# Kernel tuning notes

Measured on AMD Instinct MI355X. Metric: run time of the kernel, lower is better.

The kernel has to match this reference:

```python
import jax, jax.numpy as jnp
import numpy as np


def _run_lstm(x, h0, c0, Wih, Whh, bih, bhh):
    """Batched single-layer unidirectional LSTM (PyTorch gate order i,f,g,o).
    x: [B,T,D]; h0,c0: [B,H]; Wih: [4H,D]; Whh: [4H,H]. Returns ys [B,T,H], hT, cT."""
    def step(carry, xt):
        h, c = carry
        g = xt @ Wih.T + h @ Whh.T + bih + bhh  # [B,4H]
        i, f, gg, o = jnp.split(g, 4, axis=-1)
        c = jax.nn.sigmoid(f) * c + jax.nn.sigmoid(i) * jnp.tanh(gg)
        h = jax.nn.sigmoid(o) * jnp.tanh(c)
        return (h, c), h
    (hT, cT), ys = jax.lax.scan(step, (h0, c0), jnp.swapaxes(x, 0, 1))
    return jnp.swapaxes(ys, 0, 1), hT, cT


def setup_inputs() -> dict:
    key = jax.random.key(0)
    ks = jax.random.split(key, 16)
    B, T, D, H, L, V = 16, 256, 512, 1024, 512, 32000
    s = 0.05
    return {
        "x": jax.random.normal(ks[0], (B, T, D), jnp.float32),
        "eps": jax.random.normal(ks[1], (B, L), jnp.float32),
        "enc_Wih": jax.random.normal(ks[2], (4 * H, D), jnp.float32) * s,
        "enc_Whh": jax.random.normal(ks[3], (4 * H, H), jnp.float32) * s,
        "enc_bih": jax.random.normal(ks[4], (4 * H,), jnp.float32) * s,
        "enc_bhh": jax.random.normal(ks[5], (4 * H,), jnp.float32) * s,
        "Wmu": jax.random.normal(ks[6], (L, H), jnp.float32) * s,
        "bmu": jax.random.normal(ks[7], (L,), jnp.float32) * s,
        "Wlv": jax.random.normal(ks[8], (L, H), jnp.float32) * s,
        "blv": jax.random.normal(ks[9], (L,), jnp.float32) * s,
        "dec_Wih": jax.random.normal(ks[10], (4 * L, D), jnp.float32) * s,
        "dec_Whh": jax.random.normal(ks[11], (4 * L, L), jnp.float32) * s,
        "dec_bih": jax.random.normal(ks[12], (4 * L,), jnp.float32) * s,
        "dec_bhh": jax.random.normal(ks[13], (4 * L,), jnp.float32) * s,
        "Wout": jax.random.normal(ks[14], (V, L), jnp.float32) * s,
        "bout": jax.random.normal(ks[15], (V,), jnp.float32) * s,
    }


def reference(x, eps, enc_Wih, enc_Whh, enc_bih, enc_bhh, Wmu, bmu, Wlv, blv,
              dec_Wih, dec_Whh, dec_bih, dec_bhh, Wout, bout):
    B, T, D = x.shape
    H = enc_Whh.shape[1]
    L = Wmu.shape[0]
    # --- encode (equal-length sequences => per-sample loop == one batched LSTM) ---
    h0 = jnp.zeros((B, H), x.dtype)
    _, hT, _ = _run_lstm(x, h0, h0, enc_Wih, enc_Whh, enc_bih, enc_bhh)  # hT: [B,H]
    mu = jax.nn.relu(hT @ Wmu.T + bmu)          # [B,L]
    logvar = jax.nn.relu(hT @ Wlv.T + blv)      # [B,L]
    # --- reparameterize ---
    z = eps * jnp.exp(0.5 * logvar) + mu        # [B,L]
    # --- decode: teacher forcing, inputs shifted right by one (zeros prepended) ---
    dec_in = jnp.concatenate([jnp.zeros((B, 1, D), x.dtype), x[:, :-1]], axis=1)
    c0 = jnp.zeros((B, L), x.dtype)
    ys, _, _ = _run_lstm(dec_in, z, c0, dec_Wih, dec_Whh, dec_bih, dec_bhh)  # [B,T,L]
    logits = ys @ Wout.T + bout                 # [B,T,V]
    recons = jax.nn.softmax(logits, axis=-1)
    # match torch shapes: mus/logvars/z are [B, 1(layer), 1(per-sample batch), L]
    z4 = z[:, None, None, :]
    mu4 = mu[:, None, None, :]
    lv4 = logvar[:, None, None, :]
    return recons, z4, mu4, lv4
```

## Files before the change

kernel.cpp:

```cpp
#include <hip/hip_runtime.h>
#include <hip/hip_bf16.h>
#include <stdint.h>

#define NSLOT 32
#define GRID_LSTM 512

typedef __attribute__((ext_vector_type(4))) float f32x4;
typedef __attribute__((ext_vector_type(4))) int   i32x4;
typedef __attribute__((ext_vector_type(8))) __bf16 bf16x8;
typedef __attribute__((ext_vector_type(8))) unsigned short u16x8;

__device__ __forceinline__ float sigf(float x) { return 1.f / (1.f + __expf(-x)); }
__device__ __forceinline__ float tanhf_fast(float x) { return 1.f - 2.f / (__expf(2.f * x) + 1.f); }

__device__ __forceinline__ unsigned short f2bf(float f) {
    union { __hip_bfloat16 h; unsigned short u; } cv;
    cv.h = __float2bfloat16(f);
    return cv.u;
}
__device__ __forceinline__ float bf2f(unsigned short u) {
    union { float f; unsigned v; } c; c.v = ((unsigned)u) << 16; return c.f;
}

#define QP(x, c) __int_as_float(__builtin_amdgcn_mov_dpp(__float_as_int(x), (c), 0xF, 0xF, true))

__device__ __forceinline__ unsigned long long pack4(unsigned int h16) {
    unsigned int o4 = (unsigned int)__shfl_xor((int)h16, 4, 64);
    unsigned int p1 = h16 | (o4 << 16);
    unsigned int p2 = (unsigned int)__shfl_xor((int)p1, 8, 64);
    return (unsigned long long)p1 | ((unsigned long long)p2 << 32);
}

__device__ __forceinline__ bf16x8 load16_sc0(const unsigned short* p) {
    bf16x8 r;
    asm volatile("global_load_dwordx4 %0, %1, off sc0" : "=v"(r) : "v"(p));
    return r;
}

__device__ __forceinline__ void gld_lds16(const unsigned short* g, unsigned short* l) {
    __builtin_amdgcn_global_load_lds(
        (const __attribute__((address_space(1))) unsigned int*)g,
        (__attribute__((address_space(3))) unsigned int*)l, 16, 0, 0);
}

__device__ __forceinline__ void flag_arrive(unsigned* flags, int slot, unsigned target, int tid) {
    asm volatile("s_waitcnt vmcnt(0)" ::: "memory");
    __syncthreads();
    if (tid == 0)
        __hip_atomic_store(&flags[slot * 16], target, __ATOMIC_RELAXED, __HIP_MEMORY_SCOPE_AGENT);
}
__device__ __forceinline__ void flag_wait(unsigned* flags, unsigned target, int tid) {
    if (tid < NSLOT) {
        long sp = 0;
        while (__hip_atomic_load(&flags[tid * 16], __ATOMIC_RELAXED, __HIP_MEMORY_SCOPE_AGENT) < target) {
            if (++sp > (1L << 20)) break;
        }
    }
    __syncthreads();
    __builtin_amdgcn_sched_barrier(0);
    asm volatile("" ::: "memory");
}

__device__ __forceinline__ void register_block(unsigned* regcnt, int* s_slot, int* s_xcd, int tid) {
    if (tid == 0) {
        unsigned x;
        asm volatile("s_getreg_b32 %0, hwreg(HW_REG_XCC_ID)" : "=s"(x));
        x &= 7u;
        unsigned my = __hip_atomic_fetch_add(&regcnt[x * 16], 1u,
                                             __ATOMIC_RELAXED, __HIP_MEMORY_SCOPE_AGENT);
        *s_xcd = (int)x;
        *s_slot = (my < NSLOT) ? (int)my : -1;
    }
    __syncthreads();
}

#define CTRL_DWORDS (128 + 128 + 4096 + 4096)
__global__ void init_kernel(unsigned* ctrl) {
    int id = blockIdx.x * 256 + threadIdx.x;
    if (id < CTRL_DWORDS)
        __hip_atomic_store(&ctrl[id], 0u, __ATOMIC_RELAXED, __HIP_MEMORY_SCOPE_AGENT);
}

__global__ __launch_bounds__(256) void cvt_f32_bf16(const float* __restrict__ w,
                                                    unsigned short* __restrict__ o, int n4) {
    int id = blockIdx.x * 256 + threadIdx.x;
    if (id >= n4) return;
    f32x4 v = *(const f32x4*)(w + (size_t)id * 4);
    ushort4 r;
    r.x = f2bf(v.x); r.y = f2bf(v.y); r.z = f2bf(v.z); r.w = f2bf(v.w);
    *(ushort4*)(o + (size_t)id * 4) = r;
}

__global__ __launch_bounds__(256) void gemm_gx(
        const unsigned short* __restrict__ A, const unsigned short* __restrict__ Bm,
        unsigned short* __restrict__ outb, int N) {
    __shared__ __align__(16) unsigned short lA[128 * 32];
    __shared__ __align__(16) unsigned short lB[128 * 32];
    const int tid = threadIdx.x, bid = blockIdx.x;
    const int mt = bid & 31, nt = bid >> 5;
    const int m0 = mt * 128, n0 = nt * 128;
    const int lane = tid & 63, wvv = tid >> 6;
    const int wm = wvv >> 1, wn = wvv & 1;
    const int sr = tid >> 2, sc = (tid & 3) * 8;
    const int fr = lane & 15, kc = (lane >> 4) * 8;
    unsigned short* ldsA0 = lA + wvv * 512;
    unsigned short* ldsA1 = lA + 2048 + wvv * 512;
    unsigned short* ldsB0 = lB + wvv * 512;
    unsigned short* ldsB1 = lB + 2048 + wvv * 512;
    f32x4 acc[4][4];
    #pragma unroll
    for (int i = 0; i < 4; ++i)
        #pragma unroll
        for (int j = 0; j < 4; ++j) acc[i][j] = f32x4{0.f, 0.f, 0.f, 0.f};
    for (int k0 = 0; k0 < 512; k0 += 32) {
        __syncthreads();
        gld_lds16(A  + (size_t)(m0 + sr) * 512 + k0 + sc,        ldsA0);
        gld_lds16(A  + (size_t)(m0 + sr + 64) * 512 + k0 + sc,   ldsA1);
        gld_lds16(Bm + (size_t)(n0 + sr) * 512 + k0 + sc,        ldsB0);
        gld_lds16(Bm + (size_t)(n0 + sr + 64) * 512 + k0 + sc,   ldsB1);
        __syncthreads();
        bf16x8 af[4], bfr[4];
        #pragma unroll
        for (int mi = 0; mi < 4; ++mi)
            af[mi] = *(const bf16x8*)(lA + (wm * 64 + mi * 16 + fr) * 32 + kc);
        #pragma unroll
        for (int ni = 0; ni < 4; ++ni)
            bfr[ni] = *(const bf16x8*)(lB + (wn * 64 + ni * 16 + fr) * 32 + kc);
        #pragma unroll
        for (int mi = 0; mi < 4; ++mi)
            #pragma unroll
            for (int ni = 0; ni < 4; ++ni)
                acc[mi][ni] = __builtin_amdgcn_mfma_f32_16x16x32_bf16(af[mi], bfr[ni], acc[mi][ni], 0, 0, 0);
    }
    const int orow = (lane >> 4) * 4;
    #pragma unroll
    for (int mi = 0; mi < 4; ++mi)
        #pragma unroll
        for (int ni = 0; ni < 4; ++ni) {
            int gm = m0 + wm * 64 + mi * 16 + orow;
            int gn = n0 + wn * 64 + ni * 16 + fr;
            #pragma unroll
            for (int j = 0; j < 4; ++j)
                outb[(size_t)(gm + j) * N + gn] = f2bf(acc[mi][ni][j]);
        }
}

__global__ __launch_bounds__(256, 1) void enc_kernel(
        const float* __restrict__ Whh, const float* __restrict__ bih, const float* __restrict__ bhh,
        const unsigned short* __restrict__ gxe ,
        unsigned short* ring_e, float* __restrict__ hT, unsigned* ctrl) {
    __shared__ int s_slot, s_xcd;
    const int tid = threadIdx.x;
    register_block(ctrl , &s_slot, &s_xcd, tid);
    const int slot = s_slot, xcd = s_xcd;
    if (slot < 0) return;
    unsigned* flags = ctrl + 256 + (size_t)xcd * NSLOT * 16;
    unsigned short* ringg = ring_e + (size_t)xcd * 2 * 16384;

    const int l = tid & 63, wv = tid >> 6;
    const int n = l & 15;
    const int kch = (l >> 4) * 8;
    const int ub = slot * 32 + wv * 8;
    const int colA = (n & 3) * 1024 + ub + (n >> 2);
    const int colB = colA + 4;
    bf16x8 wA[32], wB[32];
    #pragma unroll
    for (int kk = 0; kk < 32; ++kk) {
        {
            const float* src = Whh + (size_t)colA * 1024 + kk * 32 + kch;
            f32x4 w0 = *(const f32x4*)src, w1 = *(const f32x4*)(src + 4);
            union { bf16x8 v; unsigned short u[8]; } cv;
            cv.u[0] = f2bf(w0.x); cv.u[1] = f2bf(w0.y); cv.u[2] = f2bf(w0.z); cv.u[3] = f2bf(w0.w);
            cv.u[4] = f2bf(w1.x); cv.u[5] = f2bf(w1.y); cv.u[6] = f2bf(w1.z); cv.u[7] = f2bf(w1.w);
            wA[kk] = cv.v;
        }
        {
            const float* src = Whh + (size_t)colB * 1024 + kk * 32 + kch;
            f32x4 w0 = *(const f32x4*)src, w1 = *(const f32x4*)(src + 4);
            union { bf16x8 v; unsigned short u[8]; } cv;
            cv.u[0] = f2bf(w0.x); cv.u[1] = f2bf(w0.y); cv.u[2] = f2bf(w0.z); cv.u[3] = f2bf(w0.w);
            cv.u[4] = f2bf(w1.x); cv.u[5] = f2bf(w1.y); cv.u[6] = f2bf(w1.z); cv.u[7] = f2bf(w1.w);
            wB[kk] = cv.v;
        }
    }
    const float biasA = bih[colA] + bhh[colA];
    const float biasB = bih[colB] + bhh[colB];
    float cA0 = 0.f, cA1 = 0.f, cA2 = 0.f, cA3 = 0.f;
    float cB0 = 0.f, cB1 = 0.f, cB2 = 0.f, cB3 = 0.f;
    const bool b0 = (l & 1), b1 = (l & 2);
    const bool g0lane = ((l & 3) == 0);
    const int batbase = (l >> 4) * 4;
    for (int t = 0; t < 256; ++t) {
        float gA0, gA1, gA2, gA3, gB0, gB1, gB2, gB3;
        {
            const unsigned short* g0p = gxe + ((size_t)(batbase + 0) * 256 + t) * 4096;
            const unsigned short* g1p = gxe + ((size_t)(batbase + 1) * 256 + t) * 4096;
            const unsigned short* g2p = gxe + ((size_t)(batbase + 2) * 256 + t) * 4096;
            const unsigned short* g3p = gxe + ((size_t)(batbase + 3) * 256 + t) * 4096;
            gA0 = bf2f(g0p[colA]); gB0 = bf2f(g0p[colB]);
            gA1 = bf2f(g1p[colA]); gB1 = bf2f(g1p[colB]);
            gA2 = bf2f(g2p[colA]); gB2 = bf2f(g2p[colB]);
            gA3 = bf2f(g3p[colA]); gB3 = bf2f(g3p[colB]);
        }
        f32x4 aA0 = {0.f,0.f,0.f,0.f}, aA1 = {0.f,0.f,0.f,0.f};
        f32x4 aB0 = {0.f,0.f,0.f,0.f}, aB1 = {0.f,0.f,0.f,0.f};
        if (t > 0) {
            flag_wait(flags, (unsigned)t, tid);
            const unsigned short* hb = ringg + ((t - 1) & 1) * 16384 + n * 32 + kch;
            bf16x8 ha[32];
            #pragma unroll
            for (int kk = 0; kk < 32; ++kk) ha[kk] = load16_sc0(hb + kk * 512);
            asm volatile("s_waitcnt vmcnt(0)" ::: "memory");
            __builtin_amdgcn_sched_barrier(0);
            #pragma unroll
            for (int kk = 0; kk < 16; ++kk) {
                aA0 = __builtin_amdgcn_mfma_f32_16x16x32_bf16(ha[kk],      wA[kk],      aA0, 0, 0, 0);
                aB0 = __builtin_amdgcn_mfma_f32_16x16x32_bf16(ha[kk],      wB[kk],      aB0, 0, 0, 0);
                aA1 = __builtin_amdgcn_mfma_f32_16x16x32_bf16(ha[kk + 16], wA[16 + kk], aA1, 0, 0, 0);
                aB1 = __builtin_amdgcn_mfma_f32_16x16x32_bf16(ha[kk + 16], wB[16 + kk], aB1, 0, 0, 0);
            }
        }
        unsigned short* sw = ringg + (t & 1) * 16384 + slot * 512 + wv * 8;
        #pragma unroll
        for (int j = 0; j < 4; ++j) {
            float gAj = (j == 0) ? gA0 : (j == 1) ? gA1 : (j == 2) ? gA2 : gA3;
            float gBj = (j == 0) ? gB0 : (j == 1) ? gB1 : (j == 2) ? gB2 : gB3;
            int bat = batbase + j;
            {
                float v = aA0[j] + aA1[j] + gAj + biasA;
                float vx1 = QP(v, 0xB1), vx2 = QP(v, 0x4E), vx3 = QP(v, 0x1B);
                float iv = b1 ? (b0 ? vx3 : vx2) : (b0 ? vx1 : v);
                float fv = b1 ? (b0 ? vx2 : vx3) : (b0 ? v   : vx1);
                float gv = b1 ? (b0 ? vx1 : v  ) : (b0 ? vx3 : vx2);
                float ov = b1 ? (b0 ? v   : vx1) : (b0 ? vx2 : vx3);
                float cj = (j == 0) ? cA0 : (j == 1) ? cA1 : (j == 2) ? cA2 : cA3;
                float cn = sigf(fv) * cj + sigf(iv) * tanhf_fast(gv);
                if (j == 0) cA0 = cn; else if (j == 1) cA1 = cn; else if (j == 2) cA2 = cn; else cA3 = cn;
                float h = sigf(ov) * tanhf_fast(cn);
                unsigned long long pk = pack4((unsigned)f2bf(h));
                if ((l & 15) == 0) *(unsigned long long*)(sw + bat * 32) = pk;
                if (g0lane && xcd == 0 && t == 255) hT[bat * 1024 + ub + (n >> 2)] = h;
            }
            {
                float v = aB0[j] + aB1[j] + gBj + biasB;
                float vx1 = QP(v, 0xB1), vx2 = QP(v, 0x4E), vx3 = QP(v, 0x1B);
                float iv = b1 ? (b0 ? vx3 : vx2) : (b0 ? vx1 : v);
                float fv = b1 ? (b0 ? vx2 : vx3) : (b0 ? v   : vx1);
                float gv = b1 ? (b0 ? vx1 : v  ) : (b0 ? vx3 : vx2);
                float ov = b1 ? (b0 ? v   : vx1) : (b0 ? vx2 : vx3);
                float cj = (j == 0) ? cB0 : (j == 1) ? cB1 : (j == 2) ? cB2 : cB3;
                float cn = sigf(fv) * cj + sigf(iv) * tanhf_fast(gv);
                if (j == 0) cB0 = cn; else if (j == 1) cB1 = cn; else if (j == 2) cB2 = cn; else cB3 = cn;
                float h = sigf(ov) * tanhf_fast(cn);
                unsigned long long pk = pack4((unsigned)f2bf(h));
                if ((l & 15) == 0) *(unsigned long long*)(sw + bat * 32 + 4) = pk;
                if (g0lane && xcd == 0 && t == 255) hT[bat * 1024 + ub + 4 + (n >> 2)] = h;
            }
        }
        flag_arrive(flags, slot, (unsigned)(t + 1), tid);
    }
}

__global__ __launch_bounds__(256) void mlz_kernel(
        const float* __restrict__ hT, const float* __restrict__ Wmu, const float* __restrict__ bmu,
        const float* __restrict__ Wlv, const float* __restrict__ blv, const float* __restrict__ eps,
        unsigned short* __restrict__ z_ring, float* __restrict__ out_tail) {
    int id = blockIdx.x * 256 + threadIdx.x;
    int l = id & 511, b = id >> 9;
    const float* hb = hT + b * 1024;
    const float* wm = Wmu + (size_t)l * 1024;
    const float* wl = Wlv + (size_t)l * 1024;
    float am = 0.f, al = 0.f;
    for (int k = 0; k < 256; ++k) {
        f32x4 h4 = *(const f32x4*)(hb + k * 4);
        f32x4 m4 = *(const f32x4*)(wm + k * 4);
        f32x4 l4 = *(const f32x4*)(wl + k * 4);
        am += m4.x * h4.x + m4.y * h4.y + m4.z * h4.z + m4.w * h4.w;
        al += l4.x * h4.x + l4.y * h4.y + l4.z * h4.z + l4.w * h4.w;
    }
    float mu = fmaxf(am + bmu[l], 0.f);
    float lv = fmaxf(al + blv[l], 0.f);
    float z  = eps[id] * __expf(0.5f * lv) + mu;
    z_ring[(l >> 4) * 256 + b * 16 + (l & 15)] = f2bf(z);
    out_tail[id] = z;
    out_tail[8192 + id] = mu;
    out_tail[16384 + id] = lv;
}

__global__ __launch_bounds__(256, 1) void dec_kernel(
        const float* __restrict__ Wih, const float* __restrict__ Whh,
        const float* __restrict__ bih, const float* __restrict__ bhh,
        const unsigned short* __restrict__ x_bf, const unsigned short* __restrict__ z_ring,
        unsigned short* ring_d, unsigned short* __restrict__ ys_bf, unsigned* ctrl) {
    __shared__ int s_slot, s_xcd;
    const int tid = threadIdx.x;
    register_block(ctrl + 128 , &s_slot, &s_xcd, tid);
    const int slot = s_slot, xcd = s_xcd;
    if (slot < 0) return;
    unsigned* flags = ctrl + 256 + 4096 + (size_t)xcd * NSLOT * 16;
    unsigned short* ringg = ring_d + (size_t)xcd * 2 * 8192;

    const int l = tid & 63, wv = tid >> 6;
    const int n = l & 15;
    const int kch = (l >> 4) * 8;
    const int ub = slot * 16 + wv * 4;
    const int col = (n & 3) * 512 + ub + (n >> 2);
    bf16x8 wf[32];
    #pragma unroll
    for (int kk = 0; kk < 32; ++kk) {
        const float* src = (kk < 16) ? (Wih + (size_t)col * 512 + kk * 32 + kch)
                                     : (Whh + (size_t)col * 512 + (kk - 16) * 32 + kch);
        f32x4 w0 = *(const f32x4*)src, w1 = *(const f32x4*)(src + 4);
        union { bf16x8 v; unsigned short u[8]; } cv;
        cv.u[0] = f2bf(w0.x); cv.u[1] = f2bf(w0.y); cv.u[2] = f2bf(w0.z); cv.u[3] = f2bf(w0.w);
        cv.u[4] = f2bf(w1.x); cv.u[5] = f2bf(w1.y); cv.u[6] = f2bf(w1.z); cv.u[7] = f2bf(w1.w);
        wf[kk] = cv.v;
    }
    const float bias = bih[col] + bhh[col];
    float c0 = 0.f, c1 = 0.f, c2 = 0.f, c3 = 0.f;
    const bool b0 = (l & 1), b1 = (l & 2);
    const bool g0lane = ((l & 3) == 0);
    const int batbase = (l >> 4) * 4;
    for (int t = 0; t < 256; ++t) {
        f32x4 acc0 = {0.f,0.f,0.f,0.f}, acc1 = {0.f,0.f,0.f,0.f};
        if (t > 0) {
            const unsigned short* xrow = x_bf + ((size_t)n * 256 + (t - 1)) * 512 + kch;
            #pragma unroll
            for (int kk = 0; kk < 16; ++kk) {
                bf16x8 a = *(const bf16x8*)(xrow + kk * 32);
                acc0 = __builtin_amdgcn_mfma_f32_16x16x32_bf16(a, wf[kk], acc0, 0, 0, 0);
            }
            flag_wait(flags, (unsigned)t, tid);
        }
        bf16x8 ha[16];
        if (t == 0) {
            #pragma unroll
            for (int kk = 0; kk < 16; ++kk) {
                int k = kk * 32 + kch;
                ha[kk] = *(const bf16x8*)(z_ring + (k >> 4) * 256 + n * 16 + (k & 15));
            }
        } else {
            const unsigned short* base = ringg + ((t - 1) & 1) * 8192;
            #pragma unroll
            for (int kk = 0; kk < 16; ++kk) {
                int k = kk * 32 + kch;
                ha[kk] = load16_sc0(base + (k >> 4) * 256 + n * 16 + (k & 15));
            }
            asm volatile("s_waitcnt vmcnt(0)" ::: "memory");
            __builtin_amdgcn_sched_barrier(0);
        }
        #pragma unroll
        for (int kk = 0; kk < 8; ++kk) {
            acc0 = __builtin_amdgcn_mfma_f32_16x16x32_bf16(ha[kk],     wf[16 + kk], acc0, 0, 0, 0);
            acc1 = __builtin_amdgcn_mfma_f32_16x16x32_bf16(ha[kk + 8], wf[24 + kk], acc1, 0, 0, 0);
        }
        unsigned short* sw = ringg + (t & 1) * 8192 + slot * 256 + wv * 4;
        #pragma unroll
        for (int j = 0; j < 4; ++j) {
            float v   = acc0[j] + acc1[j] + bias;
            float vx1 = QP(v, 0xB1), vx2 = QP(v, 0x4E), vx3 = QP(v, 0x1B);
            float iv = b1 ? (b0 ? vx3 : vx2) : (b0 ? vx1 : v);
            float fv = b1 ? (b0 ? vx2 : vx3) : (b0 ? v   : vx1);
            float gv = b1 ? (b0 ? vx1 : v  ) : (b0 ? vx3 : vx2);
            float ov = b1 ? (b0 ? v   : vx1) : (b0 ? vx2 : vx3);
            float cj = (j == 0) ? c0 : (j == 1) ? c1 : (j == 2) ? c2 : c3;
            float cn = sigf(fv) * cj + sigf(iv) * tanhf_fast(gv);
            if (j == 0) c0 = cn; else if (j == 1) c1 = cn; else if (j == 2) c2 = cn; else c3 = cn;
            float h = sigf(ov) * tanhf_fast(cn);
            unsigned long long pk = pack4((unsigned)f2bf(h));
            int bat = batbase + j;
            if ((l & 15) == 0) *(unsigned long long*)(sw + bat * 16) = pk;
            if (g0lane && xcd == 0)
                ys_bf[((size_t)bat * 256 + t) * 512 + ub + (n >> 2)] = f2bf(h);
        }
        flag_arrive(flags, slot, (unsigned)(t + 1), tid);
    }
}

__global__ __launch_bounds__(256) void gemm_logits(
        const unsigned short* __restrict__ A, const unsigned short* __restrict__ Wb,
        const float* __restrict__ bout, float* __restrict__ out,
        unsigned short* __restrict__ lgbf, int bfmode) {
    __shared__ __align__(16) unsigned short lA[128 * 32];
    __shared__ __align__(16) unsigned short lB[128 * 32];
    const int tid = threadIdx.x, bid = blockIdx.x;
    const int mt = bid & 31, nt = bid >> 5;
    const int m0 = mt * 128, n0 = nt * 128;
    const int lane = tid & 63, wvv = tid >> 6;
    const int wm = wvv >> 1, wn = wvv & 1;
    const int sr = tid >> 2, sc = (tid & 3) * 8;
    const int fr = lane & 15, kc = (lane >> 4) * 8;
    unsigned short* ldsA0 = lA + wvv * 512;
    unsigned short* ldsA1 = lA + 2048 + wvv * 512;
    unsigned short* ldsB0 = lB + wvv * 512;
    unsigned short* ldsB1 = lB + 2048 + wvv * 512;
    f32x4 acc[4][4];
    #pragma unroll
    for (int i = 0; i < 4; ++i)
        #pragma unroll
        for (int j = 0; j < 4; ++j) acc[i][j] = f32x4{0.f, 0.f, 0.f, 0.f};
    for (int k0 = 0; k0 < 512; k0 += 32) {
        __syncthreads();
        gld_lds16(A  + (size_t)(m0 + sr) * 512 + k0 + sc,        ldsA0);
        gld_lds16(A  + (size_t)(m0 + sr + 64) * 512 + k0 + sc,   ldsA1);
        gld_lds16(Wb + (size_t)(n0 + sr) * 512 + k0 + sc,        ldsB0);
        gld_lds16(Wb + (size_t)(n0 + sr + 64) * 512 + k0 + sc,   ldsB1);
        __syncthreads();
        bf16x8 af[4], bfr[4];
        #pragma unroll
        for (int mi = 0; mi < 4; ++mi)
            af[mi] = *(const bf16x8*)(lA + (wm * 64 + mi * 16 + fr) * 32 + kc);
        #pragma unroll
        for (int ni = 0; ni < 4; ++ni)
            bfr[ni] = *(const bf16x8*)(lB + (wn * 64 + ni * 16 + fr) * 32 + kc);
        #pragma unroll
        for (int mi = 0; mi < 4; ++mi)
            #pragma unroll
            for (int ni = 0; ni < 4; ++ni)
                acc[mi][ni] = __builtin_amdgcn_mfma_f32_16x16x32_bf16(af[mi], bfr[ni], acc[mi][ni], 0, 0, 0);
    }
    const int orow = (lane >> 4) * 4;
    #pragma unroll
    for (int mi = 0; mi < 4; ++mi)
        #pragma unroll
        for (int ni = 0; ni < 4; ++ni) {
            int gm = m0 + wm * 64 + mi * 16 + orow;
            int gn = n0 + wn * 64 + ni * 16 + fr;
            float bo = bout[gn];
            if (bfmode) {
                #pragma unroll
                for (int j = 0; j < 4; ++j)
                    lgbf[(size_t)(gm + j) * 32000 + gn] = f2bf(acc[mi][ni][j] + bo);
            } else {
                #pragma unroll
                for (int j = 0; j < 4; ++j)
                    out[(size_t)(gm + j) * 32000 + gn] = acc[mi][ni][j] + bo;
            }
        }
}

__global__ __launch_bounds__(512) void softmax_kernel(float* __restrict__ out) {
    __shared__ __align__(16) float row[32000];
    __shared__ float red[8];
    const int tid = threadIdx.x;
    float* p = out + (size_t)blockIdx.x * 32000;
    float mx = -3.4e38f;
    for (int c = tid; c < 8000; c += 512) {
        f32x4 v = *(const f32x4*)(p + c * 4);
        *(f32x4*)(row + c * 4) = v;
        mx = fmaxf(mx, fmaxf(fmaxf(v.x, v.y), fmaxf(v.z, v.w)));
    }
    #pragma unroll
    for (int o = 32; o; o >>= 1) mx = fmaxf(mx, __shfl_xor(mx, o, 64));
    if ((tid & 63) == 0) red[tid >> 6] = mx;
    __syncthreads();
    if (tid == 0) {
        float m = red[0];
        for (int i = 1; i < 8; ++i) m = fmaxf(m, red[i]);
        red[0] = m;
    }
    __syncthreads();
    mx = red[0];
    __syncthreads();
    float s = 0.f;
    for (int c = tid; c < 8000; c += 512) {
        f32x4 v = *(f32x4*)(row + c * 4);
        v.x = __expf(v.x - mx); v.y = __expf(v.y - mx);
        v.z = __expf(v.z - mx); v.w = __expf(v.w - mx);
        *(f32x4*)(row + c * 4) = v;
        s += v.x + v.y + v.z + v.w;
    }
    #pragma unroll
    for (int o = 32; o; o >>= 1) s += __shfl_xor(s, o, 64);
    if ((tid & 63) == 0) red[tid >> 6] = s;
    __syncthreads();
    if (tid == 0) {
        float t2 = 0.f;
        for (int i = 0; i < 8; ++i) t2 += red[i];
        red[0] = t2;
    }
    __syncthreads();
    float inv = 1.f / red[0];
    for (int c = tid; c < 8000; c += 512) {
        f32x4 v = *(f32x4*)(row + c * 4);
        v.x *= inv; v.y *= inv; v.z *= inv; v.w *= inv;
        *(f32x4*)(p + c * 4) = v;
    }
}

__global__ __launch_bounds__(512) void softmax_bf16(const unsigned short* __restrict__ lgbf,
                                                    float* __restrict__ out) {
    __shared__ __align__(16) float row[32000];
    __shared__ float red[8];
    const int tid = threadIdx.x;
    const unsigned short* lp = lgbf + (size_t)blockIdx.x * 32000;
    float* p = out + (size_t)blockIdx.x * 32000;
    float mx = -3.4e38f;
    for (int c = tid; c < 4000; c += 512) {
        u16x8 v = *(const u16x8*)(lp + c * 8);
        #pragma unroll
        for (int q = 0; q < 8; ++q) {
            float f = bf2f(v[q]);
            row[c * 8 + q] = f;
            mx = fmaxf(mx, f);
        }
    }
    #pragma unroll
    for (int o = 32; o; o >>= 1) mx = fmaxf(mx, __shfl_xor(mx, o, 64));
    if ((tid & 63) == 0) red[tid >> 6] = mx;
    __syncthreads();
    if (tid == 0) {
        float m = red[0];
        for (int i = 1; i < 8; ++i) m = fmaxf(m, red[i]);
        red[0] = m;
    }
    __syncthreads();
    mx = red[0];
    __syncthreads();
    float s = 0.f;
    for (int c = tid; c < 8000; c += 512) {
        f32x4 v = *(f32x4*)(row + c * 4);
        v.x = __expf(v.x - mx); v.y = __expf(v.y - mx);
        v.z = __expf(v.z - mx); v.w = __expf(v.w - mx);
        *(f32x4*)(row + c * 4) = v;
        s += v.x + v.y + v.z + v.w;
    }
    #pragma unroll
    for (int o = 32; o; o >>= 1) s += __shfl_xor(s, o, 64);
    if ((tid & 63) == 0) red[tid >> 6] = s;
    __syncthreads();
    if (tid == 0) {
        float t2 = 0.f;
        for (int i = 0; i < 8; ++i) t2 += red[i];
        red[0] = t2;
    }
    __syncthreads();
    float inv = 1.f / red[0];
    for (int c = tid; c < 8000; c += 512) {
        f32x4 v = *(f32x4*)(row + c * 4);
        v.x *= inv; v.y *= inv; v.z *= inv; v.w *= inv;
        *(f32x4*)(p + c * 4) = v;
    }
}

extern "C" void kernel_launch(void* const* d_in, const int* in_sizes, int n_in,
                              void* d_out, int out_size, void* d_ws, size_t ws_size,
                              hipStream_t stream) {
    (void)in_sizes; (void)n_in; (void)out_size;
    const float* x    = (const float*)d_in[0];
    const float* eps  = (const float*)d_in[1];
    const float* eWih = (const float*)d_in[2];
    const float* eWhh = (const float*)d_in[3];
    const float* ebih = (const float*)d_in[4];
    const float* ebhh = (const float*)d_in[5];
    const float* Wmu  = (const float*)d_in[6];
    const float* bmu  = (const float*)d_in[7];
    const float* Wlv  = (const float*)d_in[8];
    const float* blv  = (const float*)d_in[9];
    const float* dWih = (const float*)d_in[10];
    const float* dWhh = (const float*)d_in[11];
    const float* dbih = (const float*)d_in[12];
    const float* dbhh = (const float*)d_in[13];
    const float* Wout = (const float*)d_in[14];
    const float* bout = (const float*)d_in[15];
    float* out = (float*)d_out;

    char* ws = (char*)d_ws;
    unsigned* ctrl         = (unsigned*)ws;
    unsigned short* x_bf   = (unsigned short*)(ws + 65536);
    unsigned short* ysbf   = x_bf + (size_t)16 * 256 * 512;
    unsigned short* ring_e = ysbf + (size_t)4096 * 512;
    unsigned short* ring_d = ring_e + (size_t)8 * 2 * 16384;
    unsigned short* z_ring = ring_d + (size_t)8 * 2 * 8192;
    float* hT              = (float*)(z_ring + 8192);
    unsigned short* gxe    = (unsigned short*)(hT + 16384);
    unsigned short* wih_bf = ysbf;
    unsigned short* wo_bf  = gxe;
    const size_t base_end  = 65536 + 4194304 + 4194304 + 524288 + 262144 + 16384 + 65536 + 33554432;
    const size_t lg_bytes  = (size_t)4096 * 32000 * 2;
    const int bfmode       = (ws_size >= base_end + lg_bytes) ? 1 : 0;
    unsigned short* lg_bf  = (unsigned short*)(ws + base_end);

    hipLaunchKernelGGL(init_kernel, dim3(33), dim3(256), 0, stream, ctrl);
    hipLaunchKernelGGL(cvt_f32_bf16, dim3(2048), dim3(256), 0, stream, x, x_bf, 524288);
    hipLaunchKernelGGL(cvt_f32_bf16, dim3(2048), dim3(256), 0, stream, eWih, wih_bf, 524288);
    hipLaunchKernelGGL(gemm_gx, dim3(1024), dim3(256), 0, stream, x_bf, wih_bf, gxe, 4096);
    hipLaunchKernelGGL(enc_kernel, dim3(GRID_LSTM), dim3(256), 0, stream,
                       eWhh, ebih, ebhh, gxe, ring_e, hT, ctrl);
    hipLaunchKernelGGL(cvt_f32_bf16, dim3(16000), dim3(256), 0, stream, Wout, wo_bf, 4096000);
    hipLaunchKernelGGL(mlz_kernel, dim3(32), dim3(256), 0, stream,
                       hT, Wmu, bmu, Wlv, blv, eps, z_ring, out + 131072000);
    hipLaunchKernelGGL(dec_kernel, dim3(GRID_LSTM), dim3(256), 0, stream,
                       dWih, dWhh, dbih, dbhh, x_bf, z_ring, ring_d, ysbf, ctrl);
    hipLaunchKernelGGL(gemm_logits, dim3(8000), dim3(256), 0, stream,
                       ysbf, wo_bf, bout, out, lg_bf, bfmode);
    if (bfmode)
        hipLaunchKernelGGL(softmax_bf16, dim3(4096), dim3(512), 0, stream, lg_bf, out);
    else
        hipLaunchKernelGGL(softmax_kernel, dim3(4096), dim3(512), 0, stream, out);
}
```

Baseline: 3.404 ms.

## Double LSTM block width, halve slots, and convert Wout in idle blocks

```diff
diff --git a/kernel.cpp b/kernel.cpp
--- a/kernel.cpp
+++ b/kernel.cpp
@@ -2,7 +2,8 @@
 #include <hip/hip_bf16.h>
 #include <stdint.h>
 
-#define NSLOT 32
+#define NSLOT 16
+#define TPB_LSTM 512
 #define GRID_LSTM 512
 
 typedef __attribute__((ext_vector_type(4))) float f32x4;
@@ -79,6 +80,18 @@
     int id = blockIdx.x * 256 + threadIdx.x;
     if (id < CTRL_DWORDS)
         __hip_atomic_store(&ctrl[id], 0u, __ATOMIC_RELAXED, __HIP_MEMORY_SCOPE_AGENT);
+}
+
+__global__ __launch_bounds__(256) void cvt_x_wih(const float* __restrict__ x, unsigned short* __restrict__ xb,
+                                                 const float* __restrict__ w, unsigned short* __restrict__ wb) {
+    int id = blockIdx.x * 256 + threadIdx.x;
+    const float* src; unsigned short* dst; int i;
+    if (id < 524288) { src = x; dst = xb; i = id; }
+    else             { src = w; dst = wb; i = id - 524288; }
+    f32x4 v = *(const f32x4*)(src + (size_t)i * 4);
+    ushort4 r;
+    r.x = f2bf(v.x); r.y = f2bf(v.y); r.z = f2bf(v.z); r.w = f2bf(v.w);
+    *(ushort4*)(dst + (size_t)i * 4) = r;
 }
 
 __global__ __launch_bounds__(256) void cvt_f32_bf16(const float* __restrict__ w,
@@ -145,22 +158,44 @@
         }
 }
 
-__global__ __launch_bounds__(256, 1) void enc_kernel(
+__global__ __launch_bounds__(TPB_LSTM, 1) void enc_kernel(
         const float* __restrict__ Whh, const float* __restrict__ bih, const float* __restrict__ bhh,
         const unsigned short* __restrict__ gxe ,
-        unsigned short* ring_e, float* __restrict__ hT, unsigned* ctrl) {
+        unsigned short* ring_e, float* __restrict__ hT, unsigned* ctrl,
+        const float* __restrict__ Wout, unsigned short* __restrict__ wo_bf, int bfmode) {
     __shared__ int s_slot, s_xcd;
+    __shared__ int s_chunk;
     const int tid = threadIdx.x;
     register_block(ctrl , &s_slot, &s_xcd, tid);
     const int slot = s_slot, xcd = s_xcd;
-    if (slot < 0) return;
-    unsigned* flags = ctrl + 256 + (size_t)xcd * NSLOT * 16;
+    if (slot < 0) {
+        if (!bfmode) return;
+        for (;;) {
+            if (tid == 0)
+                s_chunk = (int)__hip_atomic_fetch_add(&ctrl[1], 1u,
+                                                      __ATOMIC_RELAXED, __HIP_MEMORY_SCOPE_AGENT);
+            __syncthreads();
+            int chunk = s_chunk;
+            __syncthreads();
+            if (chunk >= 1000) break;
+            size_t base = (size_t)chunk * 4096;
+            for (int i = tid; i < 4096; i += TPB_LSTM) {
+                size_t idx = base + i;
+                f32x4 v = *(const f32x4*)(Wout + idx * 4);
+                ushort4 r;
+                r.x = f2bf(v.x); r.y = f2bf(v.y); r.z = f2bf(v.z); r.w = f2bf(v.w);
+                *(ushort4*)(wo_bf + idx * 4) = r;
+            }
+        }
+        return;
+    }
+    unsigned* flags = ctrl + 256 + (size_t)xcd * 32 * 16;
     unsigned short* ringg = ring_e + (size_t)xcd * 2 * 16384;
 
     const int l = tid & 63, wv = tid >> 6;
     const int n = l & 15;
     const int kch = (l >> 4) * 8;
-    const int ub = slot * 32 + wv * 8;
+    const int ub = slot * 64 + wv * 8;
     const int colA = (n & 3) * 1024 + ub + (n >> 2);
     const int colB = colA + 4;
     bf16x8 wA[32], wB[32];
@@ -206,10 +241,13 @@
         f32x4 aB0 = {0.f,0.f,0.f,0.f}, aB1 = {0.f,0.f,0.f,0.f};
         if (t > 0) {
             flag_wait(flags, (unsigned)t, tid);
-            const unsigned short* hb = ringg + ((t - 1) & 1) * 16384 + n * 32 + kch;
+            const unsigned short* hb = ringg + ((t - 1) & 1) * 16384;
             bf16x8 ha[32];
             #pragma unroll
-            for (int kk = 0; kk < 32; ++kk) ha[kk] = load16_sc0(hb + kk * 512);
+            for (int kk = 0; kk < 32; ++kk) {
+                int ku = kk * 32 + kch;
+                ha[kk] = load16_sc0(hb + (ku >> 6) * 1024 + n * 64 + (ku & 63));
+            }
             asm volatile("s_waitcnt vmcnt(0)" ::: "memory");
             __builtin_amdgcn_sched_barrier(0);
             #pragma unroll
@@ -220,7 +258,7 @@
                 aB1 = __builtin_amdgcn_mfma_f32_16x16x32_bf16(ha[kk + 16], wB[16 + kk], aB1, 0, 0, 0);
             }
         }
-        unsigned short* sw = ringg + (t & 1) * 16384 + slot * 512 + wv * 8;
+        unsigned short* sw = ringg + (t & 1) * 16384 + slot * 1024 + wv * 8;
         #pragma unroll
         for (int j = 0; j < 4; ++j) {
             float gAj = (j == 0) ? gA0 : (j == 1) ? gA1 : (j == 2) ? gA2 : gA3;
@@ -238,7 +276,7 @@
                 if (j == 0) cA0 = cn; else if (j == 1) cA1 = cn; else if (j == 2) cA2 = cn; else cA3 = cn;
                 float h = sigf(ov) * tanhf_fast(cn);
                 unsigned long long pk = pack4((unsigned)f2bf(h));
-                if ((l & 15) == 0) *(unsigned long long*)(sw + bat * 32) = pk;
+                if ((l & 15) == 0) *(unsigned long long*)(sw + bat * 64) = pk;
                 if (g0lane && xcd == 0 && t == 255) hT[bat * 1024 + ub + (n >> 2)] = h;
             }
             {
@@ -253,7 +291,7 @@
                 if (j == 0) cB0 = cn; else if (j == 1) cB1 = cn; else if (j == 2) cB2 = cn; else cB3 = cn;
                 float h = sigf(ov) * tanhf_fast(cn);
                 unsigned long long pk = pack4((unsigned)f2bf(h));
-                if ((l & 15) == 0) *(unsigned long long*)(sw + bat * 32 + 4) = pk;
+                if ((l & 15) == 0) *(unsigned long long*)(sw + bat * 64 + 4) = pk;
                 if (g0lane && xcd == 0 && t == 255) hT[bat * 1024 + ub + 4 + (n >> 2)] = h;
             }
         }
@@ -281,13 +319,13 @@
     float mu = fmaxf(am + bmu[l], 0.f);
     float lv = fmaxf(al + blv[l], 0.f);
     float z  = eps[id] * __expf(0.5f * lv) + mu;
-    z_ring[(l >> 4) * 256 + b * 16 + (l & 15)] = f2bf(z);
+    z_ring[(l >> 5) * 512 + b * 32 + (l & 31)] = f2bf(z);
     out_tail[id] = z;
     out_tail[8192 + id] = mu;
     out_tail[16384 + id] = lv;
 }
 
-__global__ __launch_bounds__(256, 1) void dec_kernel(
+__global__ __launch_bounds__(TPB_LSTM, 1) void dec_kernel(
         const float* __restrict__ Wih, const float* __restrict__ Whh,
         const float* __restrict__ bih, const float* __restrict__ bhh,
         const unsigned short* __restrict__ x_bf, const unsigned short* __restrict__ z_ring,
@@ -297,13 +335,13 @@
     register_block(ctrl + 128 , &s_slot, &s_xcd, tid);
     const int slot = s_slot, xcd = s_xcd;
     if (slot < 0) return;
-    unsigned* flags = ctrl + 256 + 4096 + (size_t)xcd * NSLOT * 16;
+    unsigned* flags = ctrl + 256 + 4096 + (size_t)xcd * 32 * 16;
     unsigned short* ringg = ring_d + (size_t)xcd * 2 * 8192;
 
     const int l = tid & 63, wv = tid >> 6;
     const int n = l & 15;
     const int kch = (l >> 4) * 8;
-    const int ub = slot * 16 + wv * 4;
+    const int ub = slot * 32 + wv * 4;
     const int col = (n & 3) * 512 + ub + (n >> 2);
     bf16x8 wf[32];
     #pragma unroll
@@ -335,17 +373,13 @@
         bf16x8 ha[16];
         if (t == 0) {
             #pragma unroll
-            for (int kk = 0; kk < 16; ++kk) {
-                int k = kk * 32 + kch;
-                ha[kk] = *(const bf16x8*)(z_ring + (k >> 4) * 256 + n * 16 + (k & 15));
-            }
+            for (int kk = 0; kk < 16; ++kk)
+                ha[kk] = *(const bf16x8*)(z_ring + kk * 512 + n * 32 + kch);
         } else {
             const unsigned short* base = ringg + ((t - 1) & 1) * 8192;
             #pragma unroll
-            for (int kk = 0; kk < 16; ++kk) {
-                int k = kk * 32 + kch;
-                ha[kk] = load16_sc0(base + (k >> 4) * 256 + n * 16 + (k & 15));
-            }
+            for (int kk = 0; kk < 16; ++kk)
+                ha[kk] = load16_sc0(base + kk * 512 + n * 32 + kch);
             asm volatile("s_waitcnt vmcnt(0)" ::: "memory");
             __builtin_amdgcn_sched_barrier(0);
         }
@@ -354,7 +388,7 @@
             acc0 = __builtin_amdgcn_mfma_f32_16x16x32_bf16(ha[kk],     wf[16 + kk], acc0, 0, 0, 0);
             acc1 = __builtin_amdgcn_mfma_f32_16x16x32_bf16(ha[kk + 8], wf[24 + kk], acc1, 0, 0, 0);
         }
-        unsigned short* sw = ringg + (t & 1) * 8192 + slot * 256 + wv * 4;
+        unsigned short* sw = ringg + (t & 1) * 8192 + slot * 512 + wv * 4;
         #pragma unroll
         for (int j = 0; j < 4; ++j) {
             float v   = acc0[j] + acc1[j] + bias;
@@ -369,7 +403,7 @@
             float h = sigf(ov) * tanhf_fast(cn);
             unsigned long long pk = pack4((unsigned)f2bf(h));
             int bat = batbase + j;
-            if ((l & 15) == 0) *(unsigned long long*)(sw + bat * 16) = pk;
+            if ((l & 15) == 0) *(unsigned long long*)(sw + bat * 32) = pk;
             if (g0lane && xcd == 0)
                 ys_bf[((size_t)bat * 256 + t) * 512 + ub + (n >> 2)] = f2bf(h);
         }
@@ -575,22 +609,22 @@
     float* hT              = (float*)(z_ring + 8192);
     unsigned short* gxe    = (unsigned short*)(hT + 16384);
     unsigned short* wih_bf = ysbf;
-    unsigned short* wo_bf  = gxe;
     const size_t base_end  = 65536 + 4194304 + 4194304 + 524288 + 262144 + 16384 + 65536 + 33554432;
     const size_t lg_bytes  = (size_t)4096 * 32000 * 2;
     const int bfmode       = (ws_size >= base_end + lg_bytes) ? 1 : 0;
     unsigned short* lg_bf  = (unsigned short*)(ws + base_end);
+    unsigned short* wo_bf  = bfmode ? (unsigned short*)(out + (size_t)100000000) : gxe;
 
     hipLaunchKernelGGL(init_kernel, dim3(33), dim3(256), 0, stream, ctrl);
-    hipLaunchKernelGGL(cvt_f32_bf16, dim3(2048), dim3(256), 0, stream, x, x_bf, 524288);
-    hipLaunchKernelGGL(cvt_f32_bf16, dim3(2048), dim3(256), 0, stream, eWih, wih_bf, 524288);
+    hipLaunchKernelGGL(cvt_x_wih, dim3(4096), dim3(256), 0, stream, x, x_bf, eWih, wih_bf);
     hipLaunchKernelGGL(gemm_gx, dim3(1024), dim3(256), 0, stream, x_bf, wih_bf, gxe, 4096);
-    hipLaunchKernelGGL(enc_kernel, dim3(GRID_LSTM), dim3(256), 0, stream,
-                       eWhh, ebih, ebhh, gxe, ring_e, hT, ctrl);
-    hipLaunchKernelGGL(cvt_f32_bf16, dim3(16000), dim3(256), 0, stream, Wout, wo_bf, 4096000);
+    hipLaunchKernelGGL(enc_kernel, dim3(GRID_LSTM), dim3(TPB_LSTM), 0, stream,
+                       eWhh, ebih, ebhh, gxe, ring_e, hT, ctrl, Wout, wo_bf, bfmode);
+    if (!bfmode)
+        hipLaunchKernelGGL(cvt_f32_bf16, dim3(16000), dim3(256), 0, stream, Wout, wo_bf, 4096000);
     hipLaunchKernelGGL(mlz_kernel, dim3(32), dim3(256), 0, stream,
                        hT, Wmu, bmu, Wlv, blv, eps, z_ring, out + 131072000);
-    hipLaunchKernelGGL(dec_kernel, dim3(GRID_LSTM), dim3(256), 0, stream,
+    hipLaunchKernelGGL(dec_kernel, dim3(GRID_LSTM), dim3(TPB_LSTM), 0, stream,
                        dWih, dWhh, dbih, dbhh, x_bf, z_ring, ring_d, ysbf, ctrl);
     hipLaunchKernelGGL(gemm_logits, dim3(8000), dim3(256), 0, stream,
                        ysbf, wo_bf, bout, out, lg_bf, bfmode);
```

After: 8.794 ms. +158.4%, slower.

## Overlap Wout bf16 conversion with encoder LSTM using idle blocks

Applied to the files above, without the earlier changes.

```diff
diff --git a/kernel.cpp b/kernel.cpp
--- a/kernel.cpp
+++ b/kernel.cpp
@@ -79,6 +79,18 @@
     int id = blockIdx.x * 256 + threadIdx.x;
     if (id < CTRL_DWORDS)
         __hip_atomic_store(&ctrl[id], 0u, __ATOMIC_RELAXED, __HIP_MEMORY_SCOPE_AGENT);
+}
+
+__global__ __launch_bounds__(256) void cvt_x_wih(const float* __restrict__ x, unsigned short* __restrict__ xb,
+                                                 const float* __restrict__ w, unsigned short* __restrict__ wb) {
+    int id = blockIdx.x * 256 + threadIdx.x;
+    const float* src; unsigned short* dst; int i;
+    if (id < 524288) { src = x; dst = xb; i = id; }
+    else             { src = w; dst = wb; i = id - 524288; }
+    f32x4 v = *(const f32x4*)(src + (size_t)i * 4);
+    ushort4 r;
+    r.x = f2bf(v.x); r.y = f2bf(v.y); r.z = f2bf(v.z); r.w = f2bf(v.w);
+    *(ushort4*)(dst + (size_t)i * 4) = r;
 }
 
 __global__ __launch_bounds__(256) void cvt_f32_bf16(const float* __restrict__ w,
@@ -148,12 +160,34 @@
 __global__ __launch_bounds__(256, 1) void enc_kernel(
         const float* __restrict__ Whh, const float* __restrict__ bih, const float* __restrict__ bhh,
         const unsigned short* __restrict__ gxe ,
-        unsigned short* ring_e, float* __restrict__ hT, unsigned* ctrl) {
+        unsigned short* ring_e, float* __restrict__ hT, unsigned* ctrl,
+        const float* __restrict__ Wout, unsigned short* __restrict__ wo_bf, int bfmode) {
     __shared__ int s_slot, s_xcd;
+    __shared__ int s_chunk;
     const int tid = threadIdx.x;
     register_block(ctrl , &s_slot, &s_xcd, tid);
     const int slot = s_slot, xcd = s_xcd;
-    if (slot < 0) return;
+    if (slot < 0) {
+        if (!bfmode) return;
+        for (;;) {
+            if (tid == 0)
+                s_chunk = (int)__hip_atomic_fetch_add(&ctrl[1], 1u,
+                                                      __ATOMIC_RELAXED, __HIP_MEMORY_SCOPE_AGENT);
+            __syncthreads();
+            int chunk = s_chunk;
+            __syncthreads();
+            if (chunk >= 1000) break;
+            size_t base = (size_t)chunk * 4096;
+            for (int i = tid; i < 4096; i += 256) {
+                size_t idx = base + i;
+                f32x4 v = *(const f32x4*)(Wout + idx * 4);
+                ushort4 r;
+                r.x = f2bf(v.x); r.y = f2bf(v.y); r.z = f2bf(v.z); r.w = f2bf(v.w);
+                *(ushort4*)(wo_bf + idx * 4) = r;
+            }
+        }
+        return;
+    }
     unsigned* flags = ctrl + 256 + (size_t)xcd * NSLOT * 16;
     unsigned short* ringg = ring_e + (size_t)xcd * 2 * 16384;
 
@@ -575,19 +609,19 @@
     float* hT              = (float*)(z_ring + 8192);
     unsigned short* gxe    = (unsigned short*)(hT + 16384);
     unsigned short* wih_bf = ysbf;
-    unsigned short* wo_bf  = gxe;
     const size_t base_end  = 65536 + 4194304 + 4194304 + 524288 + 262144 + 16384 + 65536 + 33554432;
     const size_t lg_bytes  = (size_t)4096 * 32000 * 2;
     const int bfmode       = (ws_size >= base_end + lg_bytes) ? 1 : 0;
     unsigned short* lg_bf  = (unsigned short*)(ws + base_end);
+    unsigned short* wo_bf  = bfmode ? (unsigned short*)(out + (size_t)100000000) : gxe;
 
     hipLaunchKernelGGL(init_kernel, dim3(33), dim3(256), 0, stream, ctrl);
-    hipLaunchKernelGGL(cvt_f32_bf16, dim3(2048), dim3(256), 0, stream, x, x_bf, 524288);
-    hipLaunchKernelGGL(cvt_f32_bf16, dim3(2048), dim3(256), 0, stream, eWih, wih_bf, 524288);
+    hipLaunchKernelGGL(cvt_x_wih, dim3(4096), dim3(256), 0, stream, x, x_bf, eWih, wih_bf);
     hipLaunchKernelGGL(gemm_gx, dim3(1024), dim3(256), 0, stream, x_bf, wih_bf, gxe, 4096);
     hipLaunchKernelGGL(enc_kernel, dim3(GRID_LSTM), dim3(256), 0, stream,
-                       eWhh, ebih, ebhh, gxe, ring_e, hT, ctrl);
-    hipLaunchKernelGGL(cvt_f32_bf16, dim3(16000), dim3(256), 0, stream, Wout, wo_bf, 4096000);
+                       eWhh, ebih, ebhh, gxe, ring_e, hT, ctrl, Wout, wo_bf, bfmode);
+    if (!bfmode)
+        hipLaunchKernelGGL(cvt_f32_bf16, dim3(16000), dim3(256), 0, stream, Wout, wo_bf, 4096000);
     hipLaunchKernelGGL(mlz_kernel, dim3(32), dim3(256), 0, stream,
                        hT, Wmu, bmu, Wlv, blv, eps, z_ring, out + 131072000);
     hipLaunchKernelGGL(dec_kernel, dim3(GRID_LSTM), dim3(256), 0, stream,
```

New measurement: 3.413 ms. No clear change (+0.3%).
